# Kernel optimization log

Hardware: AMD Instinct MI355X
Metric: run time of the kernel (lower is better)

## Reference

```python
import jax, jax.numpy as jnp
import numpy as np

L, B = 4, 128
IN, CTX, ST = 512, 512, 512
R, C = 256, 256
D = IN + CTX + ST  # phi/gate input dim == write-vec input dim (state+input+context)


def _xavier(k, fan_out, fan_in, prefix=()):
    lim = float(np.sqrt(6.0 / (fan_in + fan_out)))
    return jax.random.uniform(k, prefix + (fan_out, fan_in), minval=-lim, maxval=lim, dtype=jnp.float32)


def _logit(p):
    p = np.clip(p, 1e-6, 1.0 - 1e-6)
    return float(np.log(p / (1.0 - p)))


def setup_inputs() -> dict:
    key = jax.random.key(0)
    ks = jax.random.split(key, 12)
    inp = {
        "x": jax.random.normal(ks[0], (B, IN), jnp.float32),
        "c": jax.random.normal(ks[1], (B, CTX), jnp.float32),
        "h": jax.random.normal(ks[2], (L, B, ST), jnp.float32),
        "M": jax.random.normal(ks[3], (L, B, R, C), jnp.float32),
        # per-level (non-shared) single-linear-layer gate/transition/write params
        "phi_w": _xavier(ks[4], ST, D, (L,)),
        "phi_b": jnp.zeros((L, ST), jnp.float32),
        "alpha_w": _xavier(ks[5], ST, D, (L,)),
        "alpha_b": jnp.zeros((L, ST), jnp.float32),
        "beta_w": _xavier(ks[6], ST, D, (L,)),
        "beta_b": jnp.zeros((L, ST), jnp.float32),
        "u_w": _xavier(ks[7], R, D, (L,)),
        "u_b": jnp.zeros((L, R), jnp.float32),
        "v_w": _xavier(ks[8], C, D, (L,)),
        "v_b": jnp.zeros((L, C), jnp.float32),
        "gamma_logits": jnp.full((L,), _logit(0.1), jnp.float32),
        "eta_logits": jnp.full((L,), _logit(0.01), jnp.float32),
    }
    return inp


def reference(x, c, h, M, phi_w, phi_b, alpha_w, alpha_b, beta_w, beta_b,
              u_w, u_b, v_w, v_b, gamma_logits, eta_logits):
    Ldim = h.shape[0]
    bx = jnp.broadcast_to(x[None], (Ldim,) + x.shape)  # (L,B,IN)
    bc = jnp.broadcast_to(c[None], (Ldim,) + c.shape)  # (L,B,CTX)

    # -------- gated state update (per level) --------
    gi = jnp.concatenate([bx, bc, h], axis=-1)  # (L,B,D)
    phi = jnp.einsum('lbd,lod->lbo', gi, phi_w) + phi_b[:, None, :]
    alpha = jax.nn.sigmoid(jnp.einsum('lbd,lod->lbo', gi, alpha_w) + alpha_b[:, None, :])
    beta = jax.nn.sigmoid(jnp.einsum('lbd,lod->lbo', gi, beta_w) + beta_b[:, None, :])
    h_new = alpha * jnp.tanh(phi) + beta * h  # (L,B,ST)

    # -------- outer-product EMA memory write with inter-level comm --------
    wv = jnp.concatenate([h_new, bx, bc], axis=-1)  # (L,B,D)
    u = jnp.einsum('lbd,lod->lbo', wv, u_w) + u_b[:, None, :]  # (L,B,R)
    v = jnp.einsum('lbd,lod->lbo', wv, v_w) + v_b[:, None, :]  # (L,B,C)

    # inter-level comm f = avg of neighbor memories (clamped at boundaries)
    m_up = jnp.concatenate([M[:1], M[:-1]], axis=0)
    m_dn = jnp.concatenate([M[1:], M[-1:]], axis=0)
    comm = 0.5 * (m_up + m_dn)  # (L,B,R,C)

    g = jax.nn.sigmoid(gamma_logits)[:, None, None, None]
    e = jax.nn.sigmoid(eta_logits)[:, None, None, None]
    M_new = (1.0 - g) * M + g * comm + e * jnp.einsum('lbi,lbj->lbij', u, v)
    return h_new, M_new
```

## Files before the change

kernel.cpp:

```cpp
#include <hip/hip_runtime.h>
#include <math.h>
#include <stdint.h>

constexpr int Lz  = 4;
constexpr int Bb  = 128;
constexpr int STd = 512;
constexpr int Dd  = 1536;
constexpr int Rr  = 256;
constexpr int Cc  = 256;

typedef __bf16 bf16x8 __attribute__((ext_vector_type(8)));
typedef float  f32x4  __attribute__((ext_vector_type(4)));

__device__ __forceinline__ float sigmoidf_(float v) { return 1.0f / (1.0f + expf(-v)); }

__device__ __forceinline__ uint32_t pkbf16(float a, float b) {
    uint32_t ua = __float_as_uint(a) + 0x8000u;
    uint32_t ub = __float_as_uint(b) + 0x8000u;
    return __builtin_amdgcn_perm(ub, ua, 0x07060302u);
}
__device__ __forceinline__ uint4 cvt8(const float4 lo, const float4 hi) {
    uint4 r;
    r.x = pkbf16(lo.x, lo.y); r.y = pkbf16(lo.z, lo.w);
    r.z = pkbf16(hi.x, hi.y); r.w = pkbf16(hi.z, hi.w);
    return r;
}

__global__ __launch_bounds__(256) void k_gate(
    const float* __restrict__ x, const float* __restrict__ c, const float* __restrict__ h,
    const float* __restrict__ phi_w, const float* __restrict__ phi_b,
    const float* __restrict__ alpha_w, const float* __restrict__ alpha_b,
    const float* __restrict__ beta_w, const float* __restrict__ beta_b,
    float* __restrict__ h_new)
{
    __shared__ uint32_t lds[4096];

    const int l  = blockIdx.z;
    const int b0 = blockIdx.y * 32;
    const int o0 = blockIdx.x * 32;
    const int t  = threadIdx.x;

    const int rowblk = t >> 7;
    const int kstep  = (t >> 6) & 1;
    const int ls     = t & 63;
    const int mrow   = (rowblk << 4) | (ls & 15);
    const int kd     = kstep * 32 + ((ls >> 4) << 3);
    const int slot_u = t * 4;

    const float* wrow0 = phi_w   + (size_t)(l * STd + o0 + mrow) * Dd + kd;
    const float* wrow1 = alpha_w + (size_t)(l * STd + o0 + mrow) * Dd + kd;
    const float* wrow2 = beta_w  + (size_t)(l * STd + o0 + mrow) * Dd + kd;

    const float* abase0 = x + (size_t)(b0 + mrow) * 512 + kd;
    const float* abase1 = c + (size_t)(b0 + mrow) * 512 + kd - 512;
    const float* abase2 = h + (size_t)(l * Bb + b0 + mrow) * 512 + kd - 1024;

    float4 paA0, paA1, pbA00, pbA01, pbA10, pbA11, pbA20, pbA21;
    float4 paB0, paB1, pbB00, pbB01, pbB10, pbB11, pbB20, pbB21;

    auto issueA = [&](int kk) {
        const float* p = (kk < 512 ? abase0 : (kk < 1024 ? abase1 : abase2)) + kk;
        paA0 = *(const float4*)p;  paA1 = *(const float4*)(p + 4);
        pbA00 = *(const float4*)(wrow0 + kk); pbA01 = *(const float4*)(wrow0 + kk + 4);
        pbA10 = *(const float4*)(wrow1 + kk); pbA11 = *(const float4*)(wrow1 + kk + 4);
        pbA20 = *(const float4*)(wrow2 + kk); pbA21 = *(const float4*)(wrow2 + kk + 4);
    };
    auto issueB = [&](int kk) {
        const float* p = (kk < 512 ? abase0 : (kk < 1024 ? abase1 : abase2)) + kk;
        paB0 = *(const float4*)p;  paB1 = *(const float4*)(p + 4);
        pbB00 = *(const float4*)(wrow0 + kk); pbB01 = *(const float4*)(wrow0 + kk + 4);
        pbB10 = *(const float4*)(wrow1 + kk); pbB11 = *(const float4*)(wrow1 + kk + 4);
        pbB20 = *(const float4*)(wrow2 + kk); pbB21 = *(const float4*)(wrow2 + kk + 4);
    };

    const int lane = t & 63;
    const int w    = t >> 6;
    const int m    = w >> 1;
    const int n    = w & 1;

    f32x4 acc[3] = {};

    auto mfma_step = [&]() {
        #pragma unroll
        for (int ks = 0; ks < 2; ++ks) {
            bf16x8 af  = *(bf16x8*)&lds[((m * 2 + ks) * 64 + lane) * 4];
            bf16x8 bf0 = *(bf16x8*)&lds[1024 + ((n * 2 + ks) * 64 + lane) * 4];
            bf16x8 bf1 = *(bf16x8*)&lds[2048 + ((n * 2 + ks) * 64 + lane) * 4];
            bf16x8 bf2 = *(bf16x8*)&lds[3072 + ((n * 2 + ks) * 64 + lane) * 4];
            acc[0] = __builtin_amdgcn_mfma_f32_16x16x32_bf16(af, bf0, acc[0], 0, 0, 0);
            acc[1] = __builtin_amdgcn_mfma_f32_16x16x32_bf16(af, bf1, acc[1], 0, 0, 0);
            acc[2] = __builtin_amdgcn_mfma_f32_16x16x32_bf16(af, bf2, acc[2], 0, 0, 0);
        }
    };

    issueA(0);
    issueB(64);
    for (int kk = 0; kk < Dd; kk += 128) {
        *(uint4*)&lds[slot_u]        = cvt8(paA0, paA1);
        *(uint4*)&lds[1024 + slot_u] = cvt8(pbA00, pbA01);
        *(uint4*)&lds[2048 + slot_u] = cvt8(pbA10, pbA11);
        *(uint4*)&lds[3072 + slot_u] = cvt8(pbA20, pbA21);
        __syncthreads();
        if (kk + 128 < Dd) issueA(kk + 128);
        mfma_step();
        __syncthreads();
        *(uint4*)&lds[slot_u]        = cvt8(paB0, paB1);
        *(uint4*)&lds[1024 + slot_u] = cvt8(pbB00, pbB01);
        *(uint4*)&lds[2048 + slot_u] = cvt8(pbB10, pbB11);
        *(uint4*)&lds[3072 + slot_u] = cvt8(pbB20, pbB21);
        __syncthreads();
        if (kk + 192 < Dd) issueB(kk + 192);
        mfma_step();
        __syncthreads();
    }

    const int bout = b0 + m * 16 + (lane >> 4) * 4;
    const int ocol = o0 + n * 16 + (lane & 15);
    const float pbias = phi_b[l * STd + ocol];
    const float abias = alpha_b[l * STd + ocol];
    const float bbias = beta_b[l * STd + ocol];
    #pragma unroll
    for (int r = 0; r < 4; ++r) {
        const int b = bout + r;
        float phi = acc[0][r] + pbias;
        float al  = sigmoidf_(acc[1][r] + abias);
        float be  = sigmoidf_(acc[2][r] + bbias);
        float ho  = h[(size_t)(l * Bb + b) * STd + ocol];
        h_new[(size_t)(l * Bb + b) * STd + ocol] = al * tanhf(phi) + be * ho;
    }
}

__global__ __launch_bounds__(256) void k_uv(
    const float* __restrict__ x, const float* __restrict__ c,
    const float* __restrict__ h_new,
    const float* __restrict__ u_w, const float* __restrict__ u_b,
    const float* __restrict__ v_w, const float* __restrict__ v_b,
    float* __restrict__ u_out, float* __restrict__ v_out)
{
    __shared__ uint32_t lds[2048];

    const int l   = blockIdx.z;
    const int b0  = blockIdx.y * 32;
    const int n0g = blockIdx.x * 32;
    const int t   = threadIdx.x;

    const float* W; const float* bias; float* out; int o_base;
    if (n0g < Rr) { W = u_w; bias = u_b; out = u_out; o_base = n0g; }
    else          { W = v_w; bias = v_b; out = v_out; o_base = n0g - Rr; }

    const int rowblk = t >> 7;
    const int kstep  = (t >> 6) & 1;
    const int ls     = t & 63;
    const int mrow   = (rowblk << 4) | (ls & 15);
    const int kd     = kstep * 32 + ((ls >> 4) << 3);
    const int slot_u = t * 4;

    const float* wrow = W + (size_t)(l * Rr + o_base + mrow) * Dd + kd;
    const float* abase0 = h_new + (size_t)(l * Bb + b0 + mrow) * 512 + kd;
    const float* abase1 = x + (size_t)(b0 + mrow) * 512 + kd - 512;
    const float* abase2 = c + (size_t)(b0 + mrow) * 512 + kd - 1024;

    float4 paA0, paA1, pbA0, pbA1;
    float4 paB0, paB1, pbB0, pbB1;

    auto issueA = [&](int kk) {
        const float* p = (kk < 512 ? abase0 : (kk < 1024 ? abase1 : abase2)) + kk;
        paA0 = *(const float4*)p;  paA1 = *(const float4*)(p + 4);
        pbA0 = *(const float4*)(wrow + kk); pbA1 = *(const float4*)(wrow + kk + 4);
    };
    auto issueB = [&](int kk) {
        const float* p = (kk < 512 ? abase0 : (kk < 1024 ? abase1 : abase2)) + kk;
        paB0 = *(const float4*)p;  paB1 = *(const float4*)(p + 4);
        pbB0 = *(const float4*)(wrow + kk); pbB1 = *(const float4*)(wrow + kk + 4);
    };

    const int lane = t & 63;
    const int w    = t >> 6;
    const int m    = w >> 1;
    const int n    = w & 1;

    f32x4 acc = {};

    auto mfma_step = [&]() {
        #pragma unroll
        for (int ks = 0; ks < 2; ++ks) {
            bf16x8 af = *(bf16x8*)&lds[((m * 2 + ks) * 64 + lane) * 4];
            bf16x8 bf = *(bf16x8*)&lds[1024 + ((n * 2 + ks) * 64 + lane) * 4];
            acc = __builtin_amdgcn_mfma_f32_16x16x32_bf16(af, bf, acc, 0, 0, 0);
        }
    };

    issueA(0);
    issueB(64);
    for (int kk = 0; kk < Dd; kk += 128) {
        *(uint4*)&lds[slot_u]        = cvt8(paA0, paA1);
        *(uint4*)&lds[1024 + slot_u] = cvt8(pbA0, pbA1);
        __syncthreads();
        if (kk + 128 < Dd) issueA(kk + 128);
        mfma_step();
        __syncthreads();
        *(uint4*)&lds[slot_u]        = cvt8(paB0, paB1);
        *(uint4*)&lds[1024 + slot_u] = cvt8(pbB0, pbB1);
        __syncthreads();
        if (kk + 192 < Dd) issueB(kk + 192);
        mfma_step();
        __syncthreads();
    }

    const int bout = b0 + m * 16 + (lane >> 4) * 4;
    const int ocol = o_base + n * 16 + (lane & 15);
    const float bv = bias[l * Rr + ocol];
    #pragma unroll
    for (int r = 0; r < 4; ++r) {
        out[(size_t)(l * Bb + bout + r) * Rr + ocol] = acc[r] + bv;
    }
}

__global__ __launch_bounds__(256) void k_mupd(
    const float4* __restrict__ M, const float* __restrict__ u, const float4* __restrict__ v,
    const float* __restrict__ gl, const float* __restrict__ el,
    float4* __restrict__ Mout)
{
    const int t = blockIdx.x * 256 + threadIdx.x;
    const int c4 = t & 63;
    const int r  = (t >> 6) & 255;
    const int b  = t >> 14;
    constexpr int strideL = Bb * Rr * Cc / 4;

    const float4 m0 = M[0 * strideL + t];
    const float4 m1 = M[1 * strideL + t];
    const float4 m2 = M[2 * strideL + t];
    const float4 m3 = M[3 * strideL + t];

    const int vbase = b * (Cc / 4) + c4;
    constexpr int vstride = Bb * (Cc / 4);
    const float4 v0 = v[0 * vstride + vbase];
    const float4 v1 = v[1 * vstride + vbase];
    const float4 v2 = v[2 * vstride + vbase];
    const float4 v3 = v[3 * vstride + vbase];

    const int ubase = b * Rr + r;
    constexpr int ustride = Bb * Rr;
    const float u0 = u[0 * ustride + ubase];
    const float u1 = u[1 * ustride + ubase];
    const float u2 = u[2 * ustride + ubase];
    const float u3 = u[3 * ustride + ubase];

    const float g0 = sigmoidf_(gl[0]), g1 = sigmoidf_(gl[1]);
    const float g2 = sigmoidf_(gl[2]), g3 = sigmoidf_(gl[3]);
    const float e0 = sigmoidf_(el[0]), e1 = sigmoidf_(el[1]);
    const float e2 = sigmoidf_(el[2]), e3 = sigmoidf_(el[3]);

    auto emit = [&](int l, const float4& mc, const float4& mu, const float4& md,
                    float uu, const float4& vv, float g, float e) {
        f32x4 o;
        o[0] = (1.0f - g) * mc.x + g * 0.5f * (mu.x + md.x) + e * uu * vv.x;
        o[1] = (1.0f - g) * mc.y + g * 0.5f * (mu.y + md.y) + e * uu * vv.y;
        o[2] = (1.0f - g) * mc.z + g * 0.5f * (mu.z + md.z) + e * uu * vv.z;
        o[3] = (1.0f - g) * mc.w + g * 0.5f * (mu.w + md.w) + e * uu * vv.w;
        __builtin_nontemporal_store(o, (f32x4*)&Mout[l * strideL + t]);
    };

    emit(0, m0, m0, m1, u0, v0, g0, e0);
    emit(1, m1, m0, m2, u1, v1, g1, e1);
    emit(2, m2, m1, m3, u2, v2, g2, e2);
    emit(3, m3, m2, m3, u3, v3, g3, e3);
}

extern "C" void kernel_launch(void* const* d_in, const int* in_sizes, int n_in,
                              void* d_out, int out_size, void* d_ws, size_t ws_size,
                              hipStream_t stream) {
    const float* x       = (const float*)d_in[0];
    const float* c       = (const float*)d_in[1];
    const float* h       = (const float*)d_in[2];
    const float* M       = (const float*)d_in[3];
    const float* phi_w   = (const float*)d_in[4];
    const float* phi_b   = (const float*)d_in[5];
    const float* alpha_w = (const float*)d_in[6];
    const float* alpha_b = (const float*)d_in[7];
    const float* beta_w  = (const float*)d_in[8];
    const float* beta_b  = (const float*)d_in[9];
    const float* u_w     = (const float*)d_in[10];
    const float* u_b     = (const float*)d_in[11];
    const float* v_w     = (const float*)d_in[12];
    const float* v_b     = (const float*)d_in[13];
    const float* gl      = (const float*)d_in[14];
    const float* el      = (const float*)d_in[15];

    float* out   = (float*)d_out;
    float* h_new = out;
    float* M_new = out + Lz * Bb * STd;

    float* u = (float*)d_ws;
    float* v = u + Lz * Bb * Rr;

    k_gate<<<dim3(STd / 32, Bb / 32, Lz), 256, 0, stream>>>(
        x, c, h, phi_w, phi_b, alpha_w, alpha_b, beta_w, beta_b, h_new);
    k_uv<<<dim3((Rr + Cc) / 32, Bb / 32, Lz), 256, 0, stream>>>(
        x, c, h_new, u_w, u_b, v_w, v_b, u, v);
    k_mupd<<<(Bb * Rr * Cc / 4) / 256, 256, 0, stream>>>(
        (const float4*)M, u, (const float4*)v, gl, el, (float4*)M_new);
}
```

Measured before the change: 90.94 us.

## Make memory update kernel persistent per (batch,row-chunk) with register prefetch

The M update kernel now launches 1024 blocks, each covering one batch and 32 rows and looping over 8 row-groups. The v vectors are loaded once per block, u values are staged in shared memory, and the next iteration's M loads are issued before the current compute. The aim is to cut redundant v/u loads and per-block setup and to keep more memory requests in flight. The trade-off is fewer resident waves, higher register pressure, and an extra barrier.

```diff
diff --git a/kernel.cpp b/kernel.cpp
--- a/kernel.cpp
+++ b/kernel.cpp
@@ -216,55 +216,92 @@
     }
 }
 
-__global__ __launch_bounds__(256) void k_mupd(
+__global__ __launch_bounds__(256, 4) void k_mupd(
     const float4* __restrict__ M, const float* __restrict__ u, const float4* __restrict__ v,
     const float* __restrict__ gl, const float* __restrict__ el,
     float4* __restrict__ Mout)
 {
-    const int t = blockIdx.x * 256 + threadIdx.x;
-    const int c4 = t & 63;
-    const int r  = (t >> 6) & 255;
-    const int b  = t >> 14;
-    constexpr int strideL = Bb * Rr * Cc / 4;
-
-    const float4 m0 = M[0 * strideL + t];
-    const float4 m1 = M[1 * strideL + t];
-    const float4 m2 = M[2 * strideL + t];
-    const float4 m3 = M[3 * strideL + t];
-
-    const int vbase = b * (Cc / 4) + c4;
+    constexpr int SL      = Bb * Rr * Cc / 4;
+    constexpr int ustride = Bb * Rr;
     constexpr int vstride = Bb * (Cc / 4);
-    const float4 v0 = v[0 * vstride + vbase];
-    const float4 v1 = v[1 * vstride + vbase];
-    const float4 v2 = v[2 * vstride + vbase];
-    const float4 v3 = v[3 * vstride + vbase];
-
-    const int ubase = b * Rr + r;
-    constexpr int ustride = Bb * Rr;
-    const float u0 = u[0 * ustride + ubase];
-    const float u1 = u[1 * ustride + ubase];
-    const float u2 = u[2 * ustride + ubase];
-    const float u3 = u[3 * ustride + ubase];
+    constexpr int CH      = 2048;
+
+    __shared__ float su[4][32];
+
+    const int bid = blockIdx.x;
+    const int tid = threadIdx.x;
+    const int b     = bid >> 3;
+    const int rbase = (bid & 7) * 32;
+    const int c4    = tid & 63;
+    const int w     = tid >> 6;
+
+    if (tid < 128) {
+        int l = tid >> 5, rl = tid & 31;
+        su[l][rl] = u[l * ustride + b * Rr + rbase + rl];
+    }
+
+    const int vb = b * (Cc / 4) + c4;
+    const float4 v0 = v[0 * vstride + vb];
+    const float4 v1 = v[1 * vstride + vb];
+    const float4 v2 = v[2 * vstride + vb];
+    const float4 v3 = v[3 * vstride + vb];
 
     const float g0 = sigmoidf_(gl[0]), g1 = sigmoidf_(gl[1]);
     const float g2 = sigmoidf_(gl[2]), g3 = sigmoidf_(gl[3]);
     const float e0 = sigmoidf_(el[0]), e1 = sigmoidf_(el[1]);
     const float e2 = sigmoidf_(el[2]), e3 = sigmoidf_(el[3]);
 
-    auto emit = [&](int l, const float4& mc, const float4& mu, const float4& md,
-                    float uu, const float4& vv, float g, float e) {
-        f32x4 o;
-        o[0] = (1.0f - g) * mc.x + g * 0.5f * (mu.x + md.x) + e * uu * vv.x;
-        o[1] = (1.0f - g) * mc.y + g * 0.5f * (mu.y + md.y) + e * uu * vv.y;
-        o[2] = (1.0f - g) * mc.z + g * 0.5f * (mu.z + md.z) + e * uu * vv.z;
-        o[3] = (1.0f - g) * mc.w + g * 0.5f * (mu.w + md.w) + e * uu * vv.w;
-        __builtin_nontemporal_store(o, (f32x4*)&Mout[l * strideL + t]);
-    };
-
-    emit(0, m0, m0, m1, u0, v0, g0, e0);
-    emit(1, m1, m0, m2, u1, v1, g1, e1);
-    emit(2, m2, m1, m3, u2, v2, g2, e2);
-    emit(3, m3, m2, m3, u3, v3, g3, e3);
+    __syncthreads();
+
+    const int base = bid * CH + tid;
+
+    float4 mc0 = M[0 * SL + base];
+    float4 mc1 = M[1 * SL + base];
+    float4 mc2 = M[2 * SL + base];
+    float4 mc3 = M[3 * SL + base];
+
+    #pragma unroll 1
+    for (int it = 0; it < CH / 256; ++it) {
+        const int s = base + it * 256;
+        float4 mn0, mn1, mn2, mn3;
+        if (it + 1 < CH / 256) {
+            mn0 = M[0 * SL + s + 256];
+            mn1 = M[1 * SL + s + 256];
+            mn2 = M[2 * SL + s + 256];
+            mn3 = M[3 * SL + s + 256];
+        }
+
+        const int rl = it * 4 + w;
+        const float u0 = su[0][rl], u1 = su[1][rl], u2 = su[2][rl], u3 = su[3][rl];
+
+        f32x4 o0, o1, o2, o3;
+        o0[0] = (1.0f-g0)*mc0.x + g0*0.5f*(mc0.x+mc1.x) + e0*u0*v0.x;
+        o0[1] = (1.0f-g0)*mc0.y + g0*0.5f*(mc0.y+mc1.y) + e0*u0*v0.y;
+        o0[2] = (1.0f-g0)*mc0.z + g0*0.5f*(mc0.z+mc1.z) + e0*u0*v0.z;
+        o0[3] = (1.0f-g0)*mc0.w + g0*0.5f*(mc0.w+mc1.w) + e0*u0*v0.w;
+
+        o1[0] = (1.0f-g1)*mc1.x + g1*0.5f*(mc0.x+mc2.x) + e1*u1*v1.x;
+        o1[1] = (1.0f-g1)*mc1.y + g1*0.5f*(mc0.y+mc2.y) + e1*u1*v1.y;
+        o1[2] = (1.0f-g1)*mc1.z + g1*0.5f*(mc0.z+mc2.z) + e1*u1*v1.z;
+        o1[3] = (1.0f-g1)*mc1.w + g1*0.5f*(mc0.w+mc2.w) + e1*u1*v1.w;
+
+        o2[0] = (1.0f-g2)*mc2.x + g2*0.5f*(mc1.x+mc3.x) + e2*u2*v2.x;
+        o2[1] = (1.0f-g2)*mc2.y + g2*0.5f*(mc1.y+mc3.y) + e2*u2*v2.y;
+        o2[2] = (1.0f-g2)*mc2.z + g2*0.5f*(mc1.z+mc3.z) + e2*u2*v2.z;
+        o2[3] = (1.0f-g2)*mc2.w + g2*0.5f*(mc1.w+mc3.w) + e2*u2*v2.w;
+
+        o3[0] = (1.0f-g3)*mc3.x + g3*0.5f*(mc2.x+mc3.x) + e3*u3*v3.x;
+        o3[1] = (1.0f-g3)*mc3.y + g3*0.5f*(mc2.y+mc3.y) + e3*u3*v3.y;
+        o3[2] = (1.0f-g3)*mc3.z + g3*0.5f*(mc2.z+mc3.z) + e3*u3*v3.z;
+        o3[3] = (1.0f-g3)*mc3.w + g3*0.5f*(mc2.w+mc3.w) + e3*u3*v3.w;
+
+        __builtin_nontemporal_store(o0, (f32x4*)&Mout[0 * SL + s]);
+        __builtin_nontemporal_store(o1, (f32x4*)&Mout[1 * SL + s]);
+        __builtin_nontemporal_store(o2, (f32x4*)&Mout[2 * SL + s]);
+        __builtin_nontemporal_store(o3, (f32x4*)&Mout[3 * SL + s]);
+
+        mc0 = mn0; mc1 = mn1; mc2 = mn2; mc3 = mn3;
+    }
 }
 
 extern "C" void kernel_launch(void* const* d_in, const int* in_sizes, int n_in,
@@ -298,6 +335,6 @@
         x, c, h, phi_w, phi_b, alpha_w, alpha_b, beta_w, beta_b, h_new);
     k_uv<<<dim3((Rr + Cc) / 32, Bb / 32, Lz), 256, 0, stream>>>(
         x, c, h_new, u_w, u_b, v_w, v_b, u, v);
-    k_mupd<<<(Bb * Rr * Cc / 4) / 256, 256, 0, stream>>>(
+    k_mupd<<<1024, 256, 0, stream>>>(
         (const float4*)M, u, (const float4*)v, gl, el, (float4*)M_new);
 }
```

After: 89.70 us. No clear change (-1.4%).

## Restructure memory update into per-level persistent blocks reading neighbor levels

Applied to the files above, without the earlier changes.

The M-update kernel now assigns each block one level and a chunk of 8192 float4 elements, looping over them, instead of each thread handling all four levels at one position. Each block reads its own level plus the two neighbor levels, which triples M reads at the kernel level. The kernel relies on L2/cache sharing between blocks of adjacent levels (grouped by block index interleaving and a per-level rotated iteration order) to avoid paying that in DRAM traffic. The grid shrinks from 16384 blocks to 1024 persistent-style blocks.

```diff
diff --git a/kernel.cpp b/kernel.cpp
--- a/kernel.cpp
+++ b/kernel.cpp
@@ -221,50 +221,52 @@
     const float* __restrict__ gl, const float* __restrict__ el,
     float4* __restrict__ Mout)
 {
-    const int t = blockIdx.x * 256 + threadIdx.x;
-    const int c4 = t & 63;
-    const int r  = (t >> 6) & 255;
-    const int b  = t >> 14;
-    constexpr int strideL = Bb * Rr * Cc / 4;
-
-    const float4 m0 = M[0 * strideL + t];
-    const float4 m1 = M[1 * strideL + t];
-    const float4 m2 = M[2 * strideL + t];
-    const float4 m3 = M[3 * strideL + t];
-
-    const int vbase = b * (Cc / 4) + c4;
-    constexpr int vstride = Bb * (Cc / 4);
-    const float4 v0 = v[0 * vstride + vbase];
-    const float4 v1 = v[1 * vstride + vbase];
-    const float4 v2 = v[2 * vstride + vbase];
-    const float4 v3 = v[3 * vstride + vbase];
-
-    const int ubase = b * Rr + r;
-    constexpr int ustride = Bb * Rr;
-    const float u0 = u[0 * ustride + ubase];
-    const float u1 = u[1 * ustride + ubase];
-    const float u2 = u[2 * ustride + ubase];
-    const float u3 = u[3 * ustride + ubase];
-
-    const float g0 = sigmoidf_(gl[0]), g1 = sigmoidf_(gl[1]);
-    const float g2 = sigmoidf_(gl[2]), g3 = sigmoidf_(gl[3]);
-    const float e0 = sigmoidf_(el[0]), e1 = sigmoidf_(el[1]);
-    const float e2 = sigmoidf_(el[2]), e3 = sigmoidf_(el[3]);
-
-    auto emit = [&](int l, const float4& mc, const float4& mu, const float4& md,
-                    float uu, const float4& vv, float g, float e) {
+    constexpr int SL = Bb * Rr * Cc / 4;
+    constexpr int CH = 8192;
+    constexpr int IT = CH / 256;
+
+    const int bid = blockIdx.x;
+    const int l   = (bid >> 3) & 3;
+    const int k   = (bid & 7) | ((bid >> 5) << 3);
+
+    const int lu = (l == 0) ? 0 : l - 1;
+    const int ld = (l == 3) ? 3 : l + 1;
+    const float g = sigmoidf_(gl[l]);
+    const float e = sigmoidf_(el[l]);
+
+    const int tid  = threadIdx.x;
+    const int base = k * CH;
+
+    const float*  uL = u + l * Bb * Rr;
+    const float4* vL = v + l * Bb * (Cc / 4);
+    const float4* Mc = M + (size_t)l  * SL;
+    const float4* Mu = M + (size_t)lu * SL;
+    const float4* Md = M + (size_t)ld * SL;
+    float4*       Mo = Mout + (size_t)l * SL;
+
+    #pragma unroll 2
+    for (int j = 0; j < IT; ++j) {
+        const int it = (j + l * 8) & (IT - 1);
+        const int s  = base + it * 256 + tid;
+
+        const float4 mc  = Mc[s];
+        const float4 mu_ = Mu[s];
+        const float4 md  = Md[s];
+
+        const int c4 = s & 63;
+        const int r  = (s >> 6) & 255;
+        const int b  = s >> 14;
+        const float  uu = uL[b * Rr + r];
+        const float4 vv = vL[b * (Cc / 4) + c4];
+
         f32x4 o;
-        o[0] = (1.0f - g) * mc.x + g * 0.5f * (mu.x + md.x) + e * uu * vv.x;
-        o[1] = (1.0f - g) * mc.y + g * 0.5f * (mu.y + md.y) + e * uu * vv.y;
-        o[2] = (1.0f - g) * mc.z + g * 0.5f * (mu.z + md.z) + e * uu * vv.z;
-        o[3] = (1.0f - g) * mc.w + g * 0.5f * (mu.w + md.w) + e * uu * vv.w;
-        __builtin_nontemporal_store(o, (f32x4*)&Mout[l * strideL + t]);
-    };
-
-    emit(0, m0, m0, m1, u0, v0, g0, e0);
-    emit(1, m1, m0, m2, u1, v1, g1, e1);
-    emit(2, m2, m1, m3, u2, v2, g2, e2);
-    emit(3, m3, m2, m3, u3, v3, g3, e3);
+        o[0] = (1.0f - g) * mc.x + g * 0.5f * (mu_.x + md.x) + e * uu * vv.x;
+        o[1] = (1.0f - g) * mc.y + g * 0.5f * (mu_.y + md.y) + e * uu * vv.y;
+        o[2] = (1.0f - g) * mc.z + g * 0.5f * (mu_.z + md.z) + e * uu * vv.z;
+        o[3] = (1.0f - g) * mc.w + g * 0.5f * (mu_.w + md.w) + e * uu * vv.w;
+
+        __builtin_nontemporal_store(o, (f32x4*)&Mo[s]);
+    }
 }
 
 extern "C" void kernel_launch(void* const* d_in, const int* in_sizes, int n_in,
@@ -298,6 +300,6 @@
         x, c, h, phi_w, phi_b, alpha_w, alpha_b, beta_w, beta_b, h_new);
     k_uv<<<dim3((Rr + Cc) / 32, Bb / 32, Lz), 256, 0, stream>>>(
         x, c, h_new, u_w, u_b, v_w, v_b, u, v);
-    k_mupd<<<(Bb * Rr * Cc / 4) / 256, 256, 0, stream>>>(
+    k_mupd<<<1024, 256, 0, stream>>>(
         (const float4*)M, u, (const float4*)v, gl, el, (float4*)M_new);
 }
```

Result: slower. 111.2 us (+22.3%).
